# Performance work log

Hardware: AMD Instinct MI355X
Metric: run time of the kernel (lower is better)

## Reference

```python
import jax, jax.numpy as jnp
import numpy as np

B, D, K, P = 512, 2048, 128, 5

def setup_inputs() -> dict:
    key = jax.random.key(0)
    k1, k2 = jax.random.split(key)
    x = jax.random.normal(k1, (B, D), dtype=jnp.float32)
    theta = 0.05 * jax.random.normal(k2, (D, K, P), dtype=jnp.float32)
    log_weight_scale = jnp.zeros((K, P), dtype=jnp.float32)
    bias = -jnp.ones((K,), dtype=jnp.float32)  # layer inits bias to -1
    return {"x": x, "theta": theta, "log_weight_scale": log_weight_scale, "bias": bias}

def reference(x, theta, log_weight_scale, bias):
    b = x.shape[0]
    # weight-normalized kernel: [D, K, P]
    norm = jnp.sqrt(jnp.sum(theta * theta, axis=0))            # [K, P]
    kernel = theta * (jnp.exp(log_weight_scale) / norm)[None]  # [D, K, P]
    actv = jnp.einsum('bd,dkp->bkp', x, kernel)                # [B, K, P]
    # pairwise L1 over P: [B, K, B]
    diff = jnp.abs(actv[:, :, :, None] - jnp.transpose(actv, (1, 2, 0))[None])  # [B,K,P,B]
    abs_dif = jnp.sum(diff, axis=2) + 1e6 * jnp.eye(b, dtype=x.dtype)[:, None, :]
    f = jnp.sum(jnp.exp(-abs_dif), axis=2) + bias[None, :]     # [B, K]
    return jnp.concatenate([x, f], axis=1)                     # [B, D+K]
```

## Files before the change

kernel.cpp:

```cpp
#include <hip/hip_runtime.h>
#include <math.h>

#define BSZ 512
#define DD 2048
#define KK 128
#define PP 5
#define NCOL (KK * PP)
#define OUTW (DD + KK)
#define LOG2E 1.4426950408889634f

#define KSPLIT 16
#define GM 64
#define GN 64
#define GK (DD / KSPLIT)
#define GBK 32
#define QSPLIT 8

#define WS_NORM 0
#define WS_ACTV (WS_NORM + NCOL)
#define WS_FPART (WS_ACTV + BSZ * NCOL)
#define WS_PART (WS_FPART + QSPLIT * KK * BSZ)

__global__ __launch_bounds__(256) void norm_kernel(const float* __restrict__ theta,
                                                   float* __restrict__ norm) {
    int i   = blockIdx.x * 256 + threadIdx.x;
    int col = i % NCOL;
    int seg = i / NCOL;
    const float* p = theta + (size_t)seg * 16 * NCOL + col;
    float s = 0.f;
#pragma unroll
    for (int j = 0; j < 16; ++j) {
        float v = p[(size_t)j * NCOL];
        s += v * v;
    }
    atomicAdd(&norm[col], s);
}

__global__ __launch_bounds__(256) void gemm_kernel(const float* __restrict__ x,
                                                   const float* __restrict__ theta,
                                                   float* __restrict__ part) {
    __shared__ float xT[GBK][GM];

    const int t    = threadIdx.x;
    const int lane = t & 63;
    const int wave = t >> 6;
    const int m    = blockIdx.y * GM + lane;
    const int kz   = blockIdx.z * GK;
    const int nw = __builtin_amdgcn_readfirstlane(blockIdx.x * GN + wave * 16);

    const float* xrow = x + (size_t)m * DD;

    float acc[16] = {};

    float4 v0 = *(const float4*)&xrow[kz + wave * 8];
    float4 v1 = *(const float4*)&xrow[kz + wave * 8 + 4];

    for (int kc = kz; kc < kz + GK; kc += GBK) {
        __syncthreads();
        xT[wave * 8 + 0][lane] = v0.x;
        xT[wave * 8 + 1][lane] = v0.y;
        xT[wave * 8 + 2][lane] = v0.z;
        xT[wave * 8 + 3][lane] = v0.w;
        xT[wave * 8 + 4][lane] = v1.x;
        xT[wave * 8 + 5][lane] = v1.y;
        xT[wave * 8 + 6][lane] = v1.z;
        xT[wave * 8 + 7][lane] = v1.w;
        __syncthreads();

        if (kc + GBK < kz + GK) {
            v0 = *(const float4*)&xrow[kc + GBK + wave * 8];
            v1 = *(const float4*)&xrow[kc + GBK + wave * 8 + 4];
        }

        const float* th = &theta[(size_t)kc * NCOL + nw];
#pragma unroll 4
        for (int kk = 0; kk < GBK; ++kk) {
            const float a = xT[kk][lane];
#pragma unroll
            for (int j = 0; j < 16; ++j)
                acc[j] += a * th[(size_t)kk * NCOL + j];
        }
    }

    float* dst = part + (size_t)blockIdx.z * (BSZ * NCOL) + (size_t)m * NCOL + nw;
    *(float4*)&dst[0]  = make_float4(acc[0],  acc[1],  acc[2],  acc[3]);
    *(float4*)&dst[4]  = make_float4(acc[4],  acc[5],  acc[6],  acc[7]);
    *(float4*)&dst[8]  = make_float4(acc[8],  acc[9],  acc[10], acc[11]);
    *(float4*)&dst[12] = make_float4(acc[12], acc[13], acc[14], acc[15]);
}

__global__ __launch_bounds__(256) void reduce_kernel(const float* __restrict__ part,
                                                     const float* __restrict__ norm,
                                                     const float* __restrict__ lws,
                                                     float* __restrict__ actv) {
    int i   = blockIdx.x * 256 + threadIdx.x;
    int col = i % NCOL;
    float s = 0.f;
#pragma unroll
    for (int q = 0; q < KSPLIT; ++q)
        s += part[(size_t)q * (BSZ * NCOL) + i];
    const float scale = __builtin_amdgcn_exp2f(lws[col] * LOG2E) *
                        __builtin_amdgcn_rsqf(norm[col]) * LOG2E;
    actv[i] = s * scale;
}

__global__ __launch_bounds__(128) void pairwise_kernel(const float* __restrict__ actv,
                                                       float* __restrict__ f_part) {
    const int k   = blockIdx.x;
    const int q   = blockIdx.y;
    const int tid = threadIdx.x;

    __shared__ float sB[64][8];

    for (int i = tid; i < 64 * PP; i += 128) {
        int r = i / PP;
        int p = i - r * PP;
        sB[r][p] = actv[(size_t)(q * 64 + r) * NCOL + k * PP + p];
    }

    float a[4][PP];
#pragma unroll
    for (int r = 0; r < 4; ++r) {
        const float* ap = &actv[(size_t)(tid + r * 128) * NCOL + k * PP];
#pragma unroll
        for (int p = 0; p < PP; ++p) a[r][p] = ap[p];
    }
    __syncthreads();

    float acc[4] = {0.f, 0.f, 0.f, 0.f};
#pragma unroll 2
    for (int j = 0; j < 64; ++j) {
        const float4 v  = *(const float4*)&sB[j][0];
        const float  v4 = sB[j][4];
#pragma unroll
        for (int r = 0; r < 4; ++r) {
            float s = fabsf(a[r][0] - v.x) + fabsf(a[r][1] - v.y) +
                      fabsf(a[r][2] - v.z) + fabsf(a[r][3] - v.w) +
                      fabsf(a[r][4] - v4);
            acc[r] += __builtin_amdgcn_exp2f(-s);
        }
    }

    float* fp = f_part + ((size_t)q * KK + k) * BSZ;
#pragma unroll
    for (int r = 0; r < 4; ++r)
        fp[tid + r * 128] = acc[r];
}

__global__ __launch_bounds__(256) void epilogue_kernel(const float* __restrict__ x,
                                                       const float* __restrict__ f_part,
                                                       const float* __restrict__ bias,
                                                       float* __restrict__ out) {
    const int bid = blockIdx.x;
    if (bid < 1024) {
        int i = bid * 256 + threadIdx.x;
        int r = i >> 9;
        int c = i & 511;
        float4 v = *(const float4*)&x[(size_t)r * DD + c * 4];
        *(float4*)&out[(size_t)r * OUTW + c * 4] = v;
    } else {
        int i = (bid - 1024) * 256 + threadIdx.x;
        int k = i >> 9;
        int b = i & 511;
        float s = 0.f;
#pragma unroll
        for (int q = 0; q < QSPLIT; ++q)
            s += f_part[((size_t)q * KK + k) * BSZ + b];
        out[(size_t)b * OUTW + DD + k] = s - 1.0f + bias[k];
    }
}

extern "C" void kernel_launch(void* const* d_in, const int* in_sizes, int n_in,
                              void* d_out, int out_size, void* d_ws, size_t ws_size,
                              hipStream_t stream) {
    const float* x     = (const float*)d_in[0];
    const float* theta = (const float*)d_in[1];
    const float* lws   = (const float*)d_in[2];
    const float* bias  = (const float*)d_in[3];
    float* out = (float*)d_out;

    float* ws     = (float*)d_ws;
    float* norm   = ws + WS_NORM;
    float* actv   = ws + WS_ACTV;
    float* f_part = ws + WS_FPART;
    float* part   = ws + WS_PART;

    hipMemsetAsync(norm, 0, NCOL * sizeof(float), stream);

    norm_kernel<<<320, 256, 0, stream>>>(theta, norm);
    gemm_kernel<<<dim3(NCOL / GN, BSZ / GM, KSPLIT), 256, 0, stream>>>(x, theta, part);
    reduce_kernel<<<(BSZ * NCOL) / 256, 256, 0, stream>>>(part, norm, lws, actv);
    pairwise_kernel<<<dim3(KK, QSPLIT), 128, 0, stream>>>(actv, f_part);
    epilogue_kernel<<<1280, 256, 0, stream>>>(x, f_part, bias, out);
}
```

Measured before the change: 121.9 us.

## Fuse norm, x-copy and bias init into prep kernel; atomically accumulate pairwise output

Merges the x-to-output copy, the bias initialisation of the feature columns and a shared-memory theta-norm reduction into one prep kernel that also precomputes the per-column scale. This removes the memset, the atomics on the norm and the separate epilogue launch. The pairwise kernel now atomically adds its partial sums straight into the output instead of writing f_part for a later reduction. KSPLIT is halved, which gives the GEMM fewer, longer blocks and a smaller partial buffer for reduce to read. The cost is float atomics on the output, which make the sum order nondeterministic, and less GEMM parallelism.

Result: slower. 156.7 us (+28.5%).

```diff
diff --git a/kernel.cpp b/kernel.cpp
--- a/kernel.cpp
+++ b/kernel.cpp
@@ -9,31 +9,58 @@
 #define OUTW (DD + KK)
 #define LOG2E 1.4426950408889634f
 
-#define KSPLIT 16
+#define KSPLIT 8
 #define GM 64
 #define GN 64
 #define GK (DD / KSPLIT)
 #define GBK 32
 #define QSPLIT 8
 
-#define WS_NORM 0
-#define WS_ACTV (WS_NORM + NCOL)
-#define WS_FPART (WS_ACTV + BSZ * NCOL)
-#define WS_PART (WS_FPART + QSPLIT * KK * BSZ)
+#define WS_SCALE 0
+#define WS_ACTV (WS_SCALE + NCOL)
+#define WS_PART (WS_ACTV + BSZ * NCOL)
 
-__global__ __launch_bounds__(256) void norm_kernel(const float* __restrict__ theta,
-                                                   float* __restrict__ norm) {
-    int i   = blockIdx.x * 256 + threadIdx.x;
-    int col = i % NCOL;
-    int seg = i / NCOL;
-    const float* p = theta + (size_t)seg * 16 * NCOL + col;
-    float s = 0.f;
+__global__ __launch_bounds__(256) void prep_kernel(const float* __restrict__ x,
+                                                   const float* __restrict__ theta,
+                                                   const float* __restrict__ lws,
+                                                   const float* __restrict__ bias,
+                                                   float* __restrict__ out,
+                                                   float* __restrict__ scale) {
+    const int bid = blockIdx.x;
+    const int tid = threadIdx.x;
+    if (bid < 1024) {
+        int i = bid * 256 + tid;
+        int r = i >> 9;
+        int c = i & 511;
+        float4 v = *(const float4*)&x[(size_t)r * DD + c * 4];
+        *(float4*)&out[(size_t)r * OUTW + c * 4] = v;
+    } else if (bid < 1280) {
+        int i = (bid - 1024) * 256 + tid;
+        int b = i >> 7;
+        int k = i & 127;
+        out[(size_t)b * OUTW + DD + k] = bias[k] - 1.0f;
+    } else {
+        __shared__ float snorm[16][17];
+        const int col0 = (bid - 1280) * 16;
+        const int co  = tid & 15;
+        const int seg = tid >> 4;
+        const float* p = theta + (size_t)seg * 128 * NCOL + col0 + co;
+        float s = 0.f;
+        for (int j = 0; j < 128; ++j) {
+            float v = p[(size_t)j * NCOL];
+            s += v * v;
+        }
+        snorm[seg][co] = s;
+        __syncthreads();
+        if (tid < 16) {
+            float t = 0.f;
 #pragma unroll
-    for (int j = 0; j < 16; ++j) {
-        float v = p[(size_t)j * NCOL];
-        s += v * v;
+            for (int g = 0; g < 16; ++g) t += snorm[g][tid];
+            const int col = col0 + tid;
+            scale[col] = __builtin_amdgcn_exp2f(lws[col] * LOG2E) *
+                         __builtin_amdgcn_rsqf(t) * LOG2E;
+        }
     }
-    atomicAdd(&norm[col], s);
 }
 
 __global__ __launch_bounds__(256) void gemm_kernel(const float* __restrict__ x,
@@ -90,8 +117,7 @@
 }
 
 __global__ __launch_bounds__(256) void reduce_kernel(const float* __restrict__ part,
-                                                     const float* __restrict__ norm,
-                                                     const float* __restrict__ lws,
+                                                     const float* __restrict__ scale,
                                                      float* __restrict__ actv) {
     int i   = blockIdx.x * 256 + threadIdx.x;
     int col = i % NCOL;
@@ -99,13 +125,11 @@
 #pragma unroll
     for (int q = 0; q < KSPLIT; ++q)
         s += part[(size_t)q * (BSZ * NCOL) + i];
-    const float scale = __builtin_amdgcn_exp2f(lws[col] * LOG2E) *
-                        __builtin_amdgcn_rsqf(norm[col]) * LOG2E;
-    actv[i] = s * scale;
+    actv[i] = s * scale[col];
 }
 
 __global__ __launch_bounds__(128) void pairwise_kernel(const float* __restrict__ actv,
-                                                       float* __restrict__ f_part) {
+                                                       float* __restrict__ out) {
     const int k   = blockIdx.x;
     const int q   = blockIdx.y;
     const int tid = threadIdx.x;
@@ -141,33 +165,9 @@
         }
     }
 
-    float* fp = f_part + ((size_t)q * KK + k) * BSZ;
 #pragma unroll
     for (int r = 0; r < 4; ++r)
-        fp[tid + r * 128] = acc[r];
-}
-
-__global__ __launch_bounds__(256) void epilogue_kernel(const float* __restrict__ x,
-                                                       const float* __restrict__ f_part,
-                                                       const float* __restrict__ bias,
-                                                       float* __restrict__ out) {
-    const int bid = blockIdx.x;
-    if (bid < 1024) {
-        int i = bid * 256 + threadIdx.x;
-        int r = i >> 9;
-        int c = i & 511;
-        float4 v = *(const float4*)&x[(size_t)r * DD + c * 4];
-        *(float4*)&out[(size_t)r * OUTW + c * 4] = v;
-    } else {
-        int i = (bid - 1024) * 256 + threadIdx.x;
-        int k = i >> 9;
-        int b = i & 511;
-        float s = 0.f;
-#pragma unroll
-        for (int q = 0; q < QSPLIT; ++q)
-            s += f_part[((size_t)q * KK + k) * BSZ + b];
-        out[(size_t)b * OUTW + DD + k] = s - 1.0f + bias[k];
-    }
+        atomicAdd(&out[(size_t)(tid + r * 128) * OUTW + DD + k], acc[r]);
 }
 
 extern "C" void kernel_launch(void* const* d_in, const int* in_sizes, int n_in,
@@ -179,17 +179,13 @@
     const float* bias  = (const float*)d_in[3];
     float* out = (float*)d_out;
 
-    float* ws     = (float*)d_ws;
-    float* norm   = ws + WS_NORM;
-    float* actv   = ws + WS_ACTV;
-    float* f_part = ws + WS_FPART;
-    float* part   = ws + WS_PART;
+    float* ws    = (float*)d_ws;
+    float* scale = ws + WS_SCALE;
+    float* actv  = ws + WS_ACTV;
+    float* part  = ws + WS_PART;
 
-    hipMemsetAsync(norm, 0, NCOL * sizeof(float), stream);
-
-    norm_kernel<<<320, 256, 0, stream>>>(theta, norm);
+    prep_kernel<<<1320, 256, 0, stream>>>(x, theta, lws, bias, out, scale);
     gemm_kernel<<<dim3(NCOL / GN, BSZ / GM, KSPLIT), 256, 0, stream>>>(x, theta, part);
-    reduce_kernel<<<(BSZ * NCOL) / 256, 256, 0, stream>>>(part, norm, lws, actv);
-    pairwise_kernel<<<dim3(KK, QSPLIT), 128, 0, stream>>>(actv, f_part);
-    epilogue_kernel<<<1280, 256, 0, stream>>>(x, f_part, bias, out);
+    reduce_kernel<<<(BSZ * NCOL) / 256, 256, 0, stream>>>(part, scale, actv);
+    pairwise_kernel<<<dim3(KK, QSPLIT), 128, 0, stream>>>(actv, out);
 }
```
